# Kernel tuning notes

Hardware: AMD Instinct MI355X
Metric: run time of the kernel (lower is better)

The kernel has to match this reference:

```python
import jax, jax.numpy as jnp
import numpy as np

ALPHA = 1.702   # GLU sigmoid scale
LIMIT = 7.0     # clamp limit
K = 2           # experts per token


def setup_inputs() -> dict:
    key = jax.random.key(0)
    ks = jax.random.split(key, 4)
    B, S, H, E, I = 1, 1024, 1024, 8, 1024
    return {
        "hidden_states": jax.random.normal(ks[0], (B, S, H), jnp.float32),
        "router_weight": jax.random.normal(ks[1], (E, H), jnp.float32),
        "router_bias": jnp.zeros((E,), jnp.float32),
        "gate_up_proj": jax.random.normal(ks[2], (E, H, 2 * I), jnp.float32) * 0.02,
        "gate_up_bias": jnp.zeros((E, 2 * I), jnp.float32),
        "down_proj": jax.random.normal(ks[3], (E, I, H), jnp.float32) * 0.02,
        "down_bias": jnp.zeros((E, H), jnp.float32),
    }


def reference(hidden_states, router_weight, router_bias, gate_up_proj,
              gate_up_bias, down_proj, down_bias):
    B, S, H = hidden_states.shape
    E = router_weight.shape[0]
    I = down_proj.shape[1]
    T = B * S

    flat = hidden_states.reshape(T, H)

    # Router: softmax over experts, top-K selection (weights NOT renormalized).
    logits = flat @ router_weight.T + router_bias               # [T, E]
    scores = jax.nn.softmax(logits, axis=-1)
    topk_vals, topk_idx = jax.lax.top_k(scores, K)              # [T, K]

    # Dense per-token expert weight matrix (equivalent of dispatch metadata +
    # combine * topk_weights in the tt pipeline); top-k indices are unique.
    w = jnp.zeros((T, E), scores.dtype).at[
        jnp.arange(T)[:, None], topk_idx].set(topk_vals)        # [T, E]

    # Expert MLP with clamped GLU (gpt-oss style).
    gu = jnp.einsum('th,ehf->tef', flat, gate_up_proj) + gate_up_bias  # [T,E,2I]
    gate = jnp.minimum(gu[..., :I], LIMIT)
    up = jnp.clip(gu[..., I:], -LIMIT, LIMIT)
    glu = gate * jax.nn.sigmoid(gate * ALPHA)
    act = (up + 1.0) * glu                                       # [T, E, I]

    down = jnp.einsum('tei,eih->teh', act, down_proj) + down_bias  # [T, E, H]

    # Weighted combine over selected experts.
    out = jnp.einsum('teh,te->th', down, w)
    return out.reshape(B, S, H)
```

## Files before the change

kernel.cpp:

```cpp
#include <hip/hip_runtime.h>
#include <hip/hip_bf16.h>


typedef unsigned short u16;
typedef __attribute__((ext_vector_type(8))) __bf16 bf16x8;
typedef __attribute__((ext_vector_type(4))) float f32x4;

#define T_TOK 1024
#define H_DIM 1024
#define E_NUM 8
#define I_DIM 1024
#define ALPHA 1.702f
#define LIMIT 7.0f

__device__ __forceinline__ u16 f2bf(float f) {
    unsigned u = __builtin_bit_cast(unsigned, f);
    u = (u + 0x7FFFu + ((u >> 16) & 1u)) >> 16;
    return (u16)u;
}

__device__ __forceinline__ unsigned pk2(float lo, float hi) {
#if defined(__has_builtin) && __has_builtin(__builtin_amdgcn_cvt_pk_bf16_f32)
    typedef __attribute__((ext_vector_type(2))) __bf16 bf16x2_t;
    bf16x2_t v = __builtin_amdgcn_cvt_pk_bf16_f32(lo, hi);
    return __builtin_bit_cast(unsigned, v);
#else
    return (unsigned)f2bf(lo) | ((unsigned)f2bf(hi) << 16);
#endif
}

__device__ __forceinline__ f32x4 mfma16(bf16x8 a, bf16x8 b, f32x4 c) {
    return __builtin_amdgcn_mfma_f32_16x16x32_bf16(a, b, c, 0, 0, 0);
}

__device__ __forceinline__ void gld16(const void* g, void* l) {
    __builtin_amdgcn_global_load_lds(
        (const __attribute__((address_space(1))) void*)g,
        (__attribute__((address_space(3))) void*)l, 16, 0, 0);
}

__device__ __forceinline__ void expert_range(const int* counts, int e,
                                             int& cnt, int& abase) {
    int a = 0, c = 0;
#pragma unroll
    for (int i = 0; i < E_NUM; ++i) {
        int v = counts[i];
        if (i < e) a += v;
        if (i == e) c = v;
    }
    cnt = c; abase = a;
}

__global__ __launch_bounds__(256) void k_cvt(
    const float* __restrict__ gup, const float* __restrict__ dp,
    u16* __restrict__ gupT, u16* __restrict__ dpT, int* __restrict__ counts)
{
    if (blockIdx.x == 0 && threadIdx.x < E_NUM) counts[threadIdx.x] = 0;
    const int b = blockIdx.x;
    const float* src; u16* dst; int C, k0, c0;
    if (b < 4096) {
        int e = b >> 9, t = b & 511;
        k0 = (t >> 5) * 64; c0 = (t & 31) * 64;
        src = gup + ((size_t)e << 21); dst = gupT + ((size_t)e << 21); C = 2048;
    } else {
        int b2 = b - 4096;
        int e = b2 >> 8, t = b2 & 255;
        k0 = (t >> 4) * 64; c0 = (t & 15) * 64;
        src = dp + ((size_t)e << 20); dst = dpT + ((size_t)e << 20); C = 1024;
    }
    __shared__ __align__(16) u16 Ls[64][72];
    const int tid = threadIdx.x;
    const int kq = tid >> 4, cq = tid & 15;
    float4 v0 = *(const float4*)(src + (size_t)(k0 + kq * 4 + 0) * C + c0 + cq * 4);
    float4 v1 = *(const float4*)(src + (size_t)(k0 + kq * 4 + 1) * C + c0 + cq * 4);
    float4 v2 = *(const float4*)(src + (size_t)(k0 + kq * 4 + 2) * C + c0 + cq * 4);
    float4 v3 = *(const float4*)(src + (size_t)(k0 + kq * 4 + 3) * C + c0 + cq * 4);
    const float* p0 = (const float*)&v0; const float* p1 = (const float*)&v1;
    const float* p2 = (const float*)&v2; const float* p3 = (const float*)&v3;
#pragma unroll
    for (int i = 0; i < 4; ++i) {
        *(uint2*)&Ls[cq * 4 + i][kq * 4] =
            make_uint2(pk2(p0[i], p1[i]), pk2(p2[i], p3[i]));
    }
    __syncthreads();
    const int oc = tid >> 2, och = (tid & 3) * 16;
    u16* orow = dst + (size_t)(c0 + oc) * 1024 + k0 + och;
    *(uint4*)(orow)     = *(uint4*)&Ls[oc][och];
    *(uint4*)(orow + 8) = *(uint4*)&Ls[oc][och + 8];
}

__global__ __launch_bounds__(256) void k_router(
    const float* __restrict__ x, const float* __restrict__ rw,
    const float* __restrict__ rb, const float* __restrict__ db,
    int* __restrict__ counts, int* __restrict__ tok_list,
    float* __restrict__ w_list, u16* __restrict__ xb,
    float* __restrict__ out)
{
    const int t = blockIdx.x;
    const int tid = threadIdx.x;
    const float4 xv = *(const float4*)(x + (size_t)t * H_DIM + tid * 4);

    *(uint2*)(xb + (size_t)t * H_DIM + tid * 4) =
        make_uint2(pk2(xv.x, xv.y), pk2(xv.z, xv.w));

    float p[E_NUM];
#pragma unroll
    for (int e = 0; e < E_NUM; ++e) {
        const float4 wv = *(const float4*)(rw + e * H_DIM + tid * 4);
        p[e] = xv.x * wv.x + xv.y * wv.y + xv.z * wv.z + xv.w * wv.w;
    }
#pragma unroll
    for (int off = 32; off; off >>= 1) {
#pragma unroll
        for (int e = 0; e < E_NUM; ++e) p[e] += __shfl_down(p[e], off, 64);
    }
    __shared__ float red[4][E_NUM];
    __shared__ int se[2];
    __shared__ float sw[2];
    const int lane = tid & 63, wvid = tid >> 6;
    if (lane == 0) {
#pragma unroll
        for (int e = 0; e < E_NUM; ++e) red[wvid][e] = p[e];
    }
    __syncthreads();
    if (tid == 0) {
        float lg[E_NUM];
#pragma unroll
        for (int e = 0; e < E_NUM; ++e)
            lg[e] = red[0][e] + red[1][e] + red[2][e] + red[3][e] + rb[e];
        float m1 = -1e30f, m2 = -1e30f; int i1 = 0, i2 = 0;
#pragma unroll
        for (int e = 0; e < E_NUM; ++e) {
            float l = lg[e];
            if (l > m1) { m2 = m1; i2 = i1; m1 = l; i1 = e; }
            else if (l > m2) { m2 = l; i2 = e; }
        }
        float s = 0.f;
#pragma unroll
        for (int e = 0; e < E_NUM; ++e) s += __expf(lg[e] - m1);
        const float w0 = 1.0f / s;
        const float w1 = __expf(m2 - m1) / s;
        int slot0 = atomicAdd(&counts[i1], 1);
        tok_list[i1 * T_TOK + slot0] = t;
        w_list[i1 * T_TOK + slot0] = w0;
        int slot1 = atomicAdd(&counts[i2], 1);
        tok_list[i2 * T_TOK + slot1] = t;
        w_list[i2 * T_TOK + slot1] = w1;
        se[0] = i1; se[1] = i2; sw[0] = w0; sw[1] = w1;
    }
    __syncthreads();
    const int e0 = se[0], e1 = se[1];
    const float w0 = sw[0], w1 = sw[1];
    const int c = tid * 4;
    float4 d0 = *(const float4*)(db + e0 * H_DIM + c);
    float4 d1 = *(const float4*)(db + e1 * H_DIM + c);
    float4 o;
    o.x = w0 * d0.x + w1 * d1.x;
    o.y = w0 * d0.y + w1 * d1.y;
    o.z = w0 * d0.z + w1 * d1.z;
    o.w = w0 * d0.w + w1 * d1.w;
    *(float4*)(out + (size_t)t * H_DIM + c) = o;
}

__global__ __launch_bounds__(256, 3) void k_gateup(
    const u16* __restrict__ gupT, const float* __restrict__ gub,
    const int* __restrict__ counts, const int* __restrict__ tok_list,
    const u16* __restrict__ xb, u16* __restrict__ act)
{
    const int e = blockIdx.z;
    int cnt, abase;
    expert_range(counts, e, cnt, abase);
    const int m0 = blockIdx.y * 64;
    if (m0 >= cnt) return;
    const int n0 = blockIdx.x * 64;
    const int tid = threadIdx.x;
    const int lane = tid & 63, wv = tid >> 6;
    const int fm = lane & 15, kg = lane >> 4;
    const int wm = wv >> 1, wn = wv & 1;

    __shared__ __align__(16) u16 As0[64 * 64], As1[64 * 64];
    __shared__ __align__(16) u16 Bs0[128 * 64], Bs1[128 * 64];

    const int lr = lane >> 3, lk = (lane & 7) * 8;
    const u16* gA[2];
#pragma unroll
    for (int i = 0; i < 2; ++i) {
        int row = (wv * 2 + i) * 8 + lr;
        int slot = m0 + row;
        int tok = (slot < cnt) ? tok_list[e * T_TOK + slot] : 0;
        gA[i] = xb + (size_t)tok * H_DIM + lk;
    }
    const u16* gB[4];
#pragma unroll
    for (int i = 0; i < 4; ++i) {
        int row = (wv * 4 + i) * 8 + lr;
        int col = (row < 64) ? (n0 + row) : (1024 + n0 + row - 64);
        gB[i] = gupT + ((size_t)e << 21) + (size_t)col * 1024 + lk;
    }

    f32x4 accg[2][2], accu[2][2];
#pragma unroll
    for (int m = 0; m < 2; ++m)
#pragma unroll
        for (int n = 0; n < 2; ++n) {
            accg[m][n] = (f32x4){0.f, 0.f, 0.f, 0.f};
            accu[m][n] = (f32x4){0.f, 0.f, 0.f, 0.f};
        }

#define GU_STAGE(AS, BS, KB)                                                   \
    {                                                                          \
        gld16(gA[0] + (KB), (u16*)(AS) + (wv * 2 + 0) * 512);                  \
        gld16(gA[1] + (KB), (u16*)(AS) + (wv * 2 + 1) * 512);                  \
        gld16(gB[0] + (KB), (u16*)(BS) + (wv * 4 + 0) * 512);                  \
        gld16(gB[1] + (KB), (u16*)(BS) + (wv * 4 + 1) * 512);                  \
        gld16(gB[2] + (KB), (u16*)(BS) + (wv * 4 + 2) * 512);                  \
        gld16(gB[3] + (KB), (u16*)(BS) + (wv * 4 + 3) * 512);                  \
    }
#define GU_MFMA(AS, BS)                                                        \
    {                                                                          \
        _Pragma("unroll")                                                      \
        for (int ks = 0; ks < 2; ++ks) {                                       \
            const int ko = ks * 32 + kg * 8;                                   \
            bf16x8 a0 = *(const bf16x8*)((const u16*)(AS) + (wm * 32 + fm) * 64 + ko);        \
            bf16x8 a1 = *(const bf16x8*)((const u16*)(AS) + (wm * 32 + 16 + fm) * 64 + ko);   \
            bf16x8 bg0 = *(const bf16x8*)((const u16*)(BS) + (wn * 32 + fm) * 64 + ko);       \
            bf16x8 bg1 = *(const bf16x8*)((const u16*)(BS) + (wn * 32 + 16 + fm) * 64 + ko);  \
            bf16x8 bu0 = *(const bf16x8*)((const u16*)(BS) + (64 + wn * 32 + fm) * 64 + ko);  \
            bf16x8 bu1 = *(const bf16x8*)((const u16*)(BS) + (64 + wn * 32 + 16 + fm) * 64 + ko); \
            accg[0][0] = mfma16(a0, bg0, accg[0][0]);                          \
            accg[0][1] = mfma16(a0, bg1, accg[0][1]);                          \
            accu[0][0] = mfma16(a0, bu0, accu[0][0]);                          \
            accu[0][1] = mfma16(a0, bu1, accu[0][1]);                          \
            accg[1][0] = mfma16(a1, bg0, accg[1][0]);                          \
            accg[1][1] = mfma16(a1, bg1, accg[1][1]);                          \
            accu[1][0] = mfma16(a1, bu0, accu[1][0]);                          \
            accu[1][1] = mfma16(a1, bu1, accu[1][1]);                          \
        }                                                                      \
    }

    GU_STAGE(As0, Bs0, 0);
    __syncthreads();
    for (int kb = 0; kb < H_DIM; kb += 128) {
        GU_STAGE(As1, Bs1, kb + 64);
        GU_MFMA(As0, Bs0);
        __syncthreads();
        if (kb + 128 < H_DIM) GU_STAGE(As0, Bs0, kb + 128);
        GU_MFMA(As1, Bs1);
        __syncthreads();
    }
#undef GU_STAGE
#undef GU_MFMA

#pragma unroll
    for (int m = 0; m < 2; ++m) {
#pragma unroll
        for (int r = 0; r < 4; ++r) {
            int row = wm * 32 + m * 16 + kg * 4 + r;
            int slot = m0 + row;
            if (slot >= cnt) continue;
            size_t arow = (size_t)(abase + slot) * I_DIM;
#pragma unroll
            for (int n = 0; n < 2; ++n) {
                int cn = n0 + wn * 32 + n * 16 + fm;
                float g = accg[m][n][r] + gub[e * 2048 + cn];
                float u = accu[m][n][r] + gub[e * 2048 + 1024 + cn];
                g = fminf(g, LIMIT);
                u = fminf(fmaxf(u, -LIMIT), LIMIT);
                float glu = g / (1.f + __expf(-ALPHA * g));
                act[arow + cn] = f2bf((u + 1.f) * glu);
            }
        }
    }
}

__global__ __launch_bounds__(256, 4) void k_down(
    const u16* __restrict__ dpT,
    const int* __restrict__ counts, const int* __restrict__ tok_list,
    const float* __restrict__ w_list,
    const u16* __restrict__ act, float* __restrict__ out)
{
    const int e = blockIdx.z;
    int cnt, abase;
    expert_range(counts, e, cnt, abase);
    const int m0 = blockIdx.y * 64;
    if (m0 >= cnt) return;
    const int n0 = blockIdx.x * 64;
    const int tid = threadIdx.x;
    const int lane = tid & 63, wv = tid >> 6;
    const int fm = lane & 15, kg = lane >> 4;
    const int wm = wv >> 1, wn = wv & 1;

    __shared__ __align__(16) u16 As0[64 * 64], As1[64 * 64];
    __shared__ __align__(16) u16 Bs0[64 * 64], Bs1[64 * 64];

    const int lr = lane >> 3, lk = (lane & 7) * 8;
    const u16* gA[2];
    const u16* gB[2];
#pragma unroll
    for (int i = 0; i < 2; ++i) {
        int row = (wv * 2 + i) * 8 + lr;
        gA[i] = act + (size_t)(abase + m0 + row) * I_DIM + lk;
        gB[i] = dpT + ((size_t)e << 20) + (size_t)(n0 + row) * 1024 + lk;
    }

    f32x4 acc[2][2];
#pragma unroll
    for (int m = 0; m < 2; ++m)
#pragma unroll
        for (int n = 0; n < 2; ++n) acc[m][n] = (f32x4){0.f, 0.f, 0.f, 0.f};

#define DN_STAGE(AS, BS, KB)                                                   \
    {                                                                          \
        gld16(gA[0] + (KB), (u16*)(AS) + (wv * 2 + 0) * 512);                  \
        gld16(gA[1] + (KB), (u16*)(AS) + (wv * 2 + 1) * 512);                  \
        gld16(gB[0] + (KB), (u16*)(BS) + (wv * 2 + 0) * 512);                  \
        gld16(gB[1] + (KB), (u16*)(BS) + (wv * 2 + 1) * 512);                  \
    }
#define DN_MFMA(AS, BS)                                                        \
    {                                                                          \
        _Pragma("unroll")                                                      \
        for (int ks2 = 0; ks2 < 2; ++ks2) {                                    \
            const int ko = ks2 * 32 + kg * 8;                                  \
            bf16x8 a0 = *(const bf16x8*)((const u16*)(AS) + (wm * 32 + fm) * 64 + ko);      \
            bf16x8 a1 = *(const bf16x8*)((const u16*)(AS) + (wm * 32 + 16 + fm) * 64 + ko); \
            bf16x8 b0 = *(const bf16x8*)((const u16*)(BS) + (wn * 32 + fm) * 64 + ko);      \
            bf16x8 b1 = *(const bf16x8*)((const u16*)(BS) + (wn * 32 + 16 + fm) * 64 + ko); \
            acc[0][0] = mfma16(a0, b0, acc[0][0]);                             \
            acc[0][1] = mfma16(a0, b1, acc[0][1]);                             \
            acc[1][0] = mfma16(a1, b0, acc[1][0]);                             \
            acc[1][1] = mfma16(a1, b1, acc[1][1]);                             \
        }                                                                      \
    }

    DN_STAGE(As0, Bs0, 0);
    __syncthreads();
    for (int kb = 0; kb < I_DIM; kb += 128) {
        DN_STAGE(As1, Bs1, kb + 64);
        DN_MFMA(As0, Bs0);
        __syncthreads();
        if (kb + 128 < I_DIM) DN_STAGE(As0, Bs0, kb + 128);
        DN_MFMA(As1, Bs1);
        __syncthreads();
    }
#undef DN_STAGE
#undef DN_MFMA

#pragma unroll
    for (int m = 0; m < 2; ++m) {
#pragma unroll
        for (int r = 0; r < 4; ++r) {
            int row = wm * 32 + m * 16 + kg * 4 + r;
            int slot = m0 + row;
            if (slot >= cnt) continue;
            float wgt = w_list[e * T_TOK + slot];
            int tok = tok_list[e * T_TOK + slot];
            float* orow = out + (size_t)tok * H_DIM;
#pragma unroll
            for (int n = 0; n < 2; ++n) {
                int col = n0 + wn * 32 + n * 16 + fm;
                atomicAdd(orow + col, acc[m][n][r] * wgt);
            }
        }
    }
}

extern "C" void kernel_launch(void* const* d_in, const int* in_sizes, int n_in,
                              void* d_out, int out_size, void* d_ws, size_t ws_size,
                              hipStream_t stream) {
    const float* x   = (const float*)d_in[0];
    const float* rw  = (const float*)d_in[1];
    const float* rb  = (const float*)d_in[2];
    const float* gup = (const float*)d_in[3];
    const float* gub = (const float*)d_in[4];
    const float* dp  = (const float*)d_in[5];
    const float* db  = (const float*)d_in[6];
    float* out = (float*)d_out;

    char* ws = (char*)d_ws;
    int*   counts   = (int*)(ws);
    int*   tok_list = (int*)(ws + 64);
    float* w_list   = (float*)(ws + 64 + 32768);
    u16*   xb       = (u16*)(ws + 65600);
    u16*   act      = (u16*)(ws + 65600 + 2097152);
    u16*   gupT     = (u16*)(ws + 8388608);
    u16*   dpT      = (u16*)(ws + 41943040);

    k_cvt<<<6144, 256, 0, stream>>>(gup, dp, gupT, dpT, counts);
    k_router<<<T_TOK, 256, 0, stream>>>(x, rw, rb, db, counts, tok_list, w_list,
                                        xb, out);
    k_gateup<<<dim3(16, 16, 8), 256, 0, stream>>>(gupT, gub, counts, tok_list,
                                                  xb, act);
    k_down<<<dim3(16, 16, 8), 256, 0, stream>>>(dpT, counts, tok_list, w_list,
                                                act, out);
}
```

Measured before the change: 216.1 us.

## Triple-buffer LDS with explicit vmcnt waits and XOR-swizzle in both expert GEMMs

Replaces the double-buffered K loop in the gate-up and down GEMMs with a three-stage LDS ring. Two tiles stay in flight, and hand-placed s_waitcnt vmcnt counts plus a single barrier per step replace the two __syncthreads per iteration. It also XOR-swizzles the 16-byte column chunk on both the global-to-LDS load and the MFMA fragment read, to cut LDS bank conflicts. In exchange, the extra LDS buffer lowers the launch-bounds occupancy hint for both kernels and makes correctness depend on the hand-computed outstanding-load counts.

Result: faster. 207.5 us (-4.0%).

```diff
diff --git a/kernel.cpp b/kernel.cpp
--- a/kernel.cpp
+++ b/kernel.cpp
@@ -162,7 +162,7 @@
     *(float4*)(out + (size_t)t * H_DIM + c) = o;
 }
 
-__global__ __launch_bounds__(256, 3) void k_gateup(
+__global__ __launch_bounds__(256, 2) void k_gateup(
     const u16* __restrict__ gupT, const float* __restrict__ gub,
     const int* __restrict__ counts, const int* __restrict__ tok_list,
     const u16* __restrict__ xb, u16* __restrict__ act)
@@ -178,10 +178,13 @@
     const int fm = lane & 15, kg = lane >> 4;
     const int wm = wv >> 1, wn = wv & 1;
 
-    __shared__ __align__(16) u16 As0[64 * 64], As1[64 * 64];
-    __shared__ __align__(16) u16 Bs0[128 * 64], Bs1[128 * 64];
-
-    const int lr = lane >> 3, lk = (lane & 7) * 8;
+    __shared__ __align__(16) u16 As0[64 * 64], As1[64 * 64], As2[64 * 64];
+    __shared__ __align__(16) u16 Bs0[128 * 64], Bs1[128 * 64], Bs2[128 * 64];
+    u16* const AB[3] = {As0, As1, As2};
+    u16* const BB[3] = {Bs0, Bs1, Bs2};
+
+    const int lr = lane >> 3;
+    const int lk = ((lane & 7) ^ lr) * 8;
     const u16* gA[2];
 #pragma unroll
     for (int i = 0; i < 2; ++i) {
@@ -220,7 +223,7 @@
     {                                                                          \
         _Pragma("unroll")                                                      \
         for (int ks = 0; ks < 2; ++ks) {                                       \
-            const int ko = ks * 32 + kg * 8;                                   \
+            const int ko = (((ks * 4 + kg) ^ (fm & 7)) << 3);                  \
             bf16x8 a0 = *(const bf16x8*)((const u16*)(AS) + (wm * 32 + fm) * 64 + ko);        \
             bf16x8 a1 = *(const bf16x8*)((const u16*)(AS) + (wm * 32 + 16 + fm) * 64 + ko);   \
             bf16x8 bg0 = *(const bf16x8*)((const u16*)(BS) + (wn * 32 + fm) * 64 + ko);       \
@@ -238,15 +241,15 @@
         }                                                                      \
     }
 
-    GU_STAGE(As0, Bs0, 0);
-    __syncthreads();
-    for (int kb = 0; kb < H_DIM; kb += 128) {
-        GU_STAGE(As1, Bs1, kb + 64);
-        GU_MFMA(As0, Bs0);
-        __syncthreads();
-        if (kb + 128 < H_DIM) GU_STAGE(As0, Bs0, kb + 128);
-        GU_MFMA(As1, Bs1);
-        __syncthreads();
+    GU_STAGE(AB[0], BB[0], 0);
+    GU_STAGE(AB[1], BB[1], 64);
+#pragma unroll
+    for (int p = 0; p < 16; ++p) {
+        if (p == 15) { asm volatile("s_waitcnt vmcnt(0) lgkmcnt(0)" ::: "memory"); }
+        else         { asm volatile("s_waitcnt vmcnt(6) lgkmcnt(0)" ::: "memory"); }
+        __builtin_amdgcn_s_barrier();
+        if (p + 2 < 16) GU_STAGE(AB[(p + 2) % 3], BB[(p + 2) % 3], (p + 2) * 64);
+        GU_MFMA(AB[p % 3], BB[p % 3]);
     }
 #undef GU_STAGE
 #undef GU_MFMA
@@ -273,7 +276,7 @@
     }
 }
 
-__global__ __launch_bounds__(256, 4) void k_down(
+__global__ __launch_bounds__(256, 3) void k_down(
     const u16* __restrict__ dpT,
     const int* __restrict__ counts, const int* __restrict__ tok_list,
     const float* __restrict__ w_list,
@@ -290,10 +293,13 @@
     const int fm = lane & 15, kg = lane >> 4;
     const int wm = wv >> 1, wn = wv & 1;
 
-    __shared__ __align__(16) u16 As0[64 * 64], As1[64 * 64];
-    __shared__ __align__(16) u16 Bs0[64 * 64], Bs1[64 * 64];
-
-    const int lr = lane >> 3, lk = (lane & 7) * 8;
+    __shared__ __align__(16) u16 As0[64 * 64], As1[64 * 64], As2[64 * 64];
+    __shared__ __align__(16) u16 Bs0[64 * 64], Bs1[64 * 64], Bs2[64 * 64];
+    u16* const AB[3] = {As0, As1, As2};
+    u16* const BB[3] = {Bs0, Bs1, Bs2};
+
+    const int lr = lane >> 3;
+    const int lk = ((lane & 7) ^ lr) * 8;
     const u16* gA[2];
     const u16* gB[2];
 #pragma unroll
@@ -319,8 +325,8 @@
 #define DN_MFMA(AS, BS)                                                        \
     {                                                                          \
         _Pragma("unroll")                                                      \
-        for (int ks2 = 0; ks2 < 2; ++ks2) {                                    \
-            const int ko = ks2 * 32 + kg * 8;                                  \
+        for (int ks = 0; ks < 2; ++ks) {                                       \
+            const int ko = (((ks * 4 + kg) ^ (fm & 7)) << 3);                  \
             bf16x8 a0 = *(const bf16x8*)((const u16*)(AS) + (wm * 32 + fm) * 64 + ko);      \
             bf16x8 a1 = *(const bf16x8*)((const u16*)(AS) + (wm * 32 + 16 + fm) * 64 + ko); \
             bf16x8 b0 = *(const bf16x8*)((const u16*)(BS) + (wn * 32 + fm) * 64 + ko);      \
@@ -332,15 +338,15 @@
         }                                                                      \
     }
 
-    DN_STAGE(As0, Bs0, 0);
-    __syncthreads();
-    for (int kb = 0; kb < I_DIM; kb += 128) {
-        DN_STAGE(As1, Bs1, kb + 64);
-        DN_MFMA(As0, Bs0);
-        __syncthreads();
-        if (kb + 128 < I_DIM) DN_STAGE(As0, Bs0, kb + 128);
-        DN_MFMA(As1, Bs1);
-        __syncthreads();
+    DN_STAGE(AB[0], BB[0], 0);
+    DN_STAGE(AB[1], BB[1], 64);
+#pragma unroll
+    for (int p = 0; p < 16; ++p) {
+        if (p == 15) { asm volatile("s_waitcnt vmcnt(0) lgkmcnt(0)" ::: "memory"); }
+        else         { asm volatile("s_waitcnt vmcnt(4) lgkmcnt(0)" ::: "memory"); }
+        __builtin_amdgcn_s_barrier();
+        if (p + 2 < 16) DN_STAGE(AB[(p + 2) % 3], BB[(p + 2) % 3], (p + 2) * 64);
+        DN_MFMA(AB[p % 3], BB[p % 3]);
     }
 #undef DN_STAGE
 #undef DN_MFMA
```

## Fuse fp32-to-bf16 weight conversion into expert GEMM tile loads

Applied to the files above, without the earlier changes.

Drops the separate weight transpose/convert pass, which read all fp32 expert weights and wrote bf16 transposed copies. The gate-up and down GEMMs now load fp32 weights straight from global memory into registers, pack them to bf16 and write them transposed into padded LDS tiles, using a three-stage register prefetch pipeline with explicit waitcnt and barriers. This removes a full extra write and read of the weights. In exchange, each GEMM block re-reads fp32 weights at twice the bytes, some of them several times across token tiles, uses more registers (gate-up occupancy hint lowered to 2), and gives up direct global-to-LDS loads.

New measurement: 228.0 us. 1.05x slower.

```diff
diff --git a/kernel.cpp b/kernel.cpp
--- a/kernel.cpp
+++ b/kernel.cpp
@@ -33,12 +33,6 @@
     return __builtin_amdgcn_mfma_f32_16x16x32_bf16(a, b, c, 0, 0, 0);
 }
 
-__device__ __forceinline__ void gld16(const void* g, void* l) {
-    __builtin_amdgcn_global_load_lds(
-        (const __attribute__((address_space(1))) void*)g,
-        (__attribute__((address_space(3))) void*)l, 16, 0, 0);
-}
-
 __device__ __forceinline__ void expert_range(const int* counts, int e,
                                              int& cnt, int& abase) {
     int a = 0, c = 0;
@@ -51,42 +45,8 @@
     cnt = c; abase = a;
 }
 
-__global__ __launch_bounds__(256) void k_cvt(
-    const float* __restrict__ gup, const float* __restrict__ dp,
-    u16* __restrict__ gupT, u16* __restrict__ dpT, int* __restrict__ counts)
-{
-    if (blockIdx.x == 0 && threadIdx.x < E_NUM) counts[threadIdx.x] = 0;
-    const int b = blockIdx.x;
-    const float* src; u16* dst; int C, k0, c0;
-    if (b < 4096) {
-        int e = b >> 9, t = b & 511;
-        k0 = (t >> 5) * 64; c0 = (t & 31) * 64;
-        src = gup + ((size_t)e << 21); dst = gupT + ((size_t)e << 21); C = 2048;
-    } else {
-        int b2 = b - 4096;
-        int e = b2 >> 8, t = b2 & 255;
-        k0 = (t >> 4) * 64; c0 = (t & 15) * 64;
-        src = dp + ((size_t)e << 20); dst = dpT + ((size_t)e << 20); C = 1024;
-    }
-    __shared__ __align__(16) u16 Ls[64][72];
-    const int tid = threadIdx.x;
-    const int kq = tid >> 4, cq = tid & 15;
-    float4 v0 = *(const float4*)(src + (size_t)(k0 + kq * 4 + 0) * C + c0 + cq * 4);
-    float4 v1 = *(const float4*)(src + (size_t)(k0 + kq * 4 + 1) * C + c0 + cq * 4);
-    float4 v2 = *(const float4*)(src + (size_t)(k0 + kq * 4 + 2) * C + c0 + cq * 4);
-    float4 v3 = *(const float4*)(src + (size_t)(k0 + kq * 4 + 3) * C + c0 + cq * 4);
-    const float* p0 = (const float*)&v0; const float* p1 = (const float*)&v1;
-    const float* p2 = (const float*)&v2; const float* p3 = (const float*)&v3;
-#pragma unroll
-    for (int i = 0; i < 4; ++i) {
-        *(uint2*)&Ls[cq * 4 + i][kq * 4] =
-            make_uint2(pk2(p0[i], p1[i]), pk2(p2[i], p3[i]));
-    }
-    __syncthreads();
-    const int oc = tid >> 2, och = (tid & 3) * 16;
-    u16* orow = dst + (size_t)(c0 + oc) * 1024 + k0 + och;
-    *(uint4*)(orow)     = *(uint4*)&Ls[oc][och];
-    *(uint4*)(orow + 8) = *(uint4*)&Ls[oc][och + 8];
+__global__ void k_zero(int* counts) {
+    if (threadIdx.x < E_NUM) counts[threadIdx.x] = 0;
 }
 
 __global__ __launch_bounds__(256) void k_router(
@@ -162,8 +122,8 @@
     *(float4*)(out + (size_t)t * H_DIM + c) = o;
 }
 
-__global__ __launch_bounds__(256, 3) void k_gateup(
-    const u16* __restrict__ gupT, const float* __restrict__ gub,
+__global__ __launch_bounds__(256, 2) void k_gateup(
+    const float* __restrict__ gup, const float* __restrict__ gub,
     const int* __restrict__ counts, const int* __restrict__ tok_list,
     const u16* __restrict__ xb, u16* __restrict__ act)
 {
@@ -178,25 +138,19 @@
     const int fm = lane & 15, kg = lane >> 4;
     const int wm = wv >> 1, wn = wv & 1;
 
-    __shared__ __align__(16) u16 As0[64 * 64], As1[64 * 64];
-    __shared__ __align__(16) u16 Bs0[128 * 64], Bs1[128 * 64];
-
-    const int lr = lane >> 3, lk = (lane & 7) * 8;
-    const u16* gA[2];
-#pragma unroll
-    for (int i = 0; i < 2; ++i) {
-        int row = (wv * 2 + i) * 8 + lr;
-        int slot = m0 + row;
-        int tok = (slot < cnt) ? tok_list[e * T_TOK + slot] : 0;
-        gA[i] = xb + (size_t)tok * H_DIM + lk;
-    }
-    const u16* gB[4];
-#pragma unroll
-    for (int i = 0; i < 4; ++i) {
-        int row = (wv * 4 + i) * 8 + lr;
-        int col = (row < 64) ? (n0 + row) : (1024 + n0 + row - 64);
-        gB[i] = gupT + ((size_t)e << 21) + (size_t)col * 1024 + lk;
-    }
+    __shared__ __align__(16) u16 As[2][64 * 72];
+    __shared__ __align__(16) u16 Bs[2][128 * 72];
+    unsigned* const Bs32[2] = {(unsigned*)Bs[0], (unsigned*)Bs[1]};
+
+    const int kq = tid >> 3, cq = tid & 7;
+    const int arow = tid >> 2, kc = tid & 3;
+    const int aslot = m0 + arow;
+    const int atok = (aslot < cnt) ? tok_list[e * T_TOK + aslot] : 0;
+    const u16* gA = xb + (size_t)atok * H_DIM;
+    const float* gB = gup + ((size_t)e << 21) + n0;
+
+    float4 Bf[2][2][2][2];
+    uint4 Aa[2][2];
 
     f32x4 accg[2][2], accu[2][2];
 #pragma unroll
@@ -207,26 +161,47 @@
             accu[m][n] = (f32x4){0.f, 0.f, 0.f, 0.f};
         }
 
-#define GU_STAGE(AS, BS, KB)                                                   \
-    {                                                                          \
-        gld16(gA[0] + (KB), (u16*)(AS) + (wv * 2 + 0) * 512);                  \
-        gld16(gA[1] + (KB), (u16*)(AS) + (wv * 2 + 1) * 512);                  \
-        gld16(gB[0] + (KB), (u16*)(BS) + (wv * 4 + 0) * 512);                  \
-        gld16(gB[1] + (KB), (u16*)(BS) + (wv * 4 + 1) * 512);                  \
-        gld16(gB[2] + (KB), (u16*)(BS) + (wv * 4 + 2) * 512);                  \
-        gld16(gB[3] + (KB), (u16*)(BS) + (wv * 4 + 3) * 512);                  \
-    }
-#define GU_MFMA(AS, BS)                                                        \
+#define GU_LOADS(S, KB)                                                        \
+    {                                                                          \
+        _Pragma("unroll")                                                      \
+        for (int sub = 0; sub < 2; ++sub)                                      \
+        _Pragma("unroll")                                                      \
+        for (int half = 0; half < 2; ++half)                                   \
+        _Pragma("unroll")                                                      \
+        for (int j = 0; j < 2; ++j)                                            \
+            Bf[S][sub][half][j] = *(const float4*)(gB +                        \
+                (size_t)((KB) + 2 * kq + j) * 2048 + half * 1024 +             \
+                sub * 32 + cq * 4);                                            \
+        Aa[S][0] = *(const uint4*)(gA + (KB) + kc * 16);                       \
+        Aa[S][1] = *(const uint4*)(gA + (KB) + kc * 16 + 8);                   \
+    }
+#define GU_WRITE(S, BUF)                                                       \
+    {                                                                          \
+        _Pragma("unroll")                                                      \
+        for (int sub = 0; sub < 2; ++sub)                                      \
+        _Pragma("unroll")                                                      \
+        for (int half = 0; half < 2; ++half)                                   \
+        _Pragma("unroll")                                                      \
+        for (int c = 0; c < 4; ++c) {                                          \
+            const float* j0 = (const float*)&Bf[S][sub][half][0];              \
+            const float* j1 = (const float*)&Bf[S][sub][half][1];              \
+            Bs32[BUF][(half * 64 + sub * 32 + cq * 4 + c) * 36 + kq] =         \
+                pk2(j0[c], j1[c]);                                             \
+        }                                                                      \
+        *(uint4*)&As[BUF][arow * 72 + kc * 16]     = Aa[S][0];                 \
+        *(uint4*)&As[BUF][arow * 72 + kc * 16 + 8] = Aa[S][1];                 \
+    }
+#define GU_MFMA(BUF)                                                           \
     {                                                                          \
         _Pragma("unroll")                                                      \
         for (int ks = 0; ks < 2; ++ks) {                                       \
             const int ko = ks * 32 + kg * 8;                                   \
-            bf16x8 a0 = *(const bf16x8*)((const u16*)(AS) + (wm * 32 + fm) * 64 + ko);        \
-            bf16x8 a1 = *(const bf16x8*)((const u16*)(AS) + (wm * 32 + 16 + fm) * 64 + ko);   \
-            bf16x8 bg0 = *(const bf16x8*)((const u16*)(BS) + (wn * 32 + fm) * 64 + ko);       \
-            bf16x8 bg1 = *(const bf16x8*)((const u16*)(BS) + (wn * 32 + 16 + fm) * 64 + ko);  \
-            bf16x8 bu0 = *(const bf16x8*)((const u16*)(BS) + (64 + wn * 32 + fm) * 64 + ko);  \
-            bf16x8 bu1 = *(const bf16x8*)((const u16*)(BS) + (64 + wn * 32 + 16 + fm) * 64 + ko); \
+            bf16x8 a0 = *(const bf16x8*)&As[BUF][(wm * 32 + fm) * 72 + ko];        \
+            bf16x8 a1 = *(const bf16x8*)&As[BUF][(wm * 32 + 16 + fm) * 72 + ko];   \
+            bf16x8 bg0 = *(const bf16x8*)&Bs[BUF][(wn * 32 + fm) * 72 + ko];       \
+            bf16x8 bg1 = *(const bf16x8*)&Bs[BUF][(wn * 32 + 16 + fm) * 72 + ko];  \
+            bf16x8 bu0 = *(const bf16x8*)&Bs[BUF][(64 + wn * 32 + fm) * 72 + ko];  \
+            bf16x8 bu1 = *(const bf16x8*)&Bs[BUF][(64 + wn * 32 + 16 + fm) * 72 + ko]; \
             accg[0][0] = mfma16(a0, bg0, accg[0][0]);                          \
             accg[0][1] = mfma16(a0, bg1, accg[0][1]);                          \
             accu[0][0] = mfma16(a0, bu0, accu[0][0]);                          \
@@ -238,17 +213,28 @@
         }                                                                      \
     }
 
-    GU_STAGE(As0, Bs0, 0);
-    __syncthreads();
-    for (int kb = 0; kb < H_DIM; kb += 128) {
-        GU_STAGE(As1, Bs1, kb + 64);
-        GU_MFMA(As0, Bs0);
-        __syncthreads();
-        if (kb + 128 < H_DIM) GU_STAGE(As0, Bs0, kb + 128);
-        GU_MFMA(As1, Bs1);
-        __syncthreads();
-    }
-#undef GU_STAGE
+    GU_LOADS(0, 0);
+    GU_LOADS(1, 64);
+    asm volatile("s_waitcnt vmcnt(10)" ::: "memory");
+    GU_WRITE(0, 0);
+    GU_LOADS(0, 128);
+    asm volatile("s_waitcnt lgkmcnt(0)" ::: "memory");
+    __builtin_amdgcn_s_barrier();
+
+#pragma unroll
+    for (int t = 0; t < 16; ++t) {
+        if (t <= 13)      { asm volatile("s_waitcnt vmcnt(10)" ::: "memory"); }
+        else if (t == 14) { asm volatile("s_waitcnt vmcnt(0)"  ::: "memory"); }
+        if (t + 1 < 16) GU_WRITE((t + 1) & 1, (t + 1) & 1);
+        if (t + 3 < 16) GU_LOADS((t + 3) & 1, (t + 3) * 64);
+        GU_MFMA(t & 1);
+        if (t + 1 < 16) {
+            asm volatile("s_waitcnt lgkmcnt(0)" ::: "memory");
+            __builtin_amdgcn_s_barrier();
+        }
+    }
+#undef GU_LOADS
+#undef GU_WRITE
 #undef GU_MFMA
 
 #pragma unroll
@@ -258,7 +244,7 @@
             int row = wm * 32 + m * 16 + kg * 4 + r;
             int slot = m0 + row;
             if (slot >= cnt) continue;
-            size_t arow = (size_t)(abase + slot) * I_DIM;
+            size_t arowo = (size_t)(abase + slot) * I_DIM;
 #pragma unroll
             for (int n = 0; n < 2; ++n) {
                 int cn = n0 + wn * 32 + n * 16 + fm;
@@ -267,14 +253,14 @@
                 g = fminf(g, LIMIT);
                 u = fminf(fmaxf(u, -LIMIT), LIMIT);
                 float glu = g / (1.f + __expf(-ALPHA * g));
-                act[arow + cn] = f2bf((u + 1.f) * glu);
+                act[arowo + cn] = f2bf((u + 1.f) * glu);
             }
         }
     }
 }
 
 __global__ __launch_bounds__(256, 4) void k_down(
-    const u16* __restrict__ dpT,
+    const float* __restrict__ dp,
     const int* __restrict__ counts, const int* __restrict__ tok_list,
     const float* __restrict__ w_list,
     const u16* __restrict__ act, float* __restrict__ out)
@@ -290,18 +276,17 @@
     const int fm = lane & 15, kg = lane >> 4;
     const int wm = wv >> 1, wn = wv & 1;
 
-    __shared__ __align__(16) u16 As0[64 * 64], As1[64 * 64];
-    __shared__ __align__(16) u16 Bs0[64 * 64], Bs1[64 * 64];
-
-    const int lr = lane >> 3, lk = (lane & 7) * 8;
-    const u16* gA[2];
-    const u16* gB[2];
-#pragma unroll
-    for (int i = 0; i < 2; ++i) {
-        int row = (wv * 2 + i) * 8 + lr;
-        gA[i] = act + (size_t)(abase + m0 + row) * I_DIM + lk;
-        gB[i] = dpT + ((size_t)e << 20) + (size_t)(n0 + row) * 1024 + lk;
-    }
+    __shared__ __align__(16) u16 As[2][64 * 72];
+    __shared__ __align__(16) u16 Bs[2][64 * 72];
+    unsigned* const Bs32[2] = {(unsigned*)Bs[0], (unsigned*)Bs[1]};
+
+    const int kq = tid >> 3, cq = tid & 7;
+    const int arow = tid >> 2, kc = tid & 3;
+    const u16* gA = act + (size_t)(abase + m0 + arow) * I_DIM;
+    const float* gB = dp + ((size_t)e << 20) + n0;
+
+    float4 Bf[2][2][2];
+    uint4 Aa[2][2];
 
     f32x4 acc[2][2];
 #pragma unroll
@@ -309,22 +294,39 @@
 #pragma unroll
         for (int n = 0; n < 2; ++n) acc[m][n] = (f32x4){0.f, 0.f, 0.f, 0.f};
 
-#define DN_STAGE(AS, BS, KB)                                                   \
-    {                                                                          \
-        gld16(gA[0] + (KB), (u16*)(AS) + (wv * 2 + 0) * 512);                  \
-        gld16(gA[1] + (KB), (u16*)(AS) + (wv * 2 + 1) * 512);                  \
-        gld16(gB[0] + (KB), (u16*)(BS) + (wv * 2 + 0) * 512);                  \
-        gld16(gB[1] + (KB), (u16*)(BS) + (wv * 2 + 1) * 512);                  \
-    }
-#define DN_MFMA(AS, BS)                                                        \
-    {                                                                          \
-        _Pragma("unroll")                                                      \
-        for (int ks2 = 0; ks2 < 2; ++ks2) {                                    \
-            const int ko = ks2 * 32 + kg * 8;                                  \
-            bf16x8 a0 = *(const bf16x8*)((const u16*)(AS) + (wm * 32 + fm) * 64 + ko);      \
-            bf16x8 a1 = *(const bf16x8*)((const u16*)(AS) + (wm * 32 + 16 + fm) * 64 + ko); \
-            bf16x8 b0 = *(const bf16x8*)((const u16*)(BS) + (wn * 32 + fm) * 64 + ko);      \
-            bf16x8 b1 = *(const bf16x8*)((const u16*)(BS) + (wn * 32 + 16 + fm) * 64 + ko); \
+#define DN_LOADS(S, KB)                                                        \
+    {                                                                          \
+        _Pragma("unroll")                                                      \
+        for (int sub = 0; sub < 2; ++sub)                                      \
+        _Pragma("unroll")                                                      \
+        for (int j = 0; j < 2; ++j)                                            \
+            Bf[S][sub][j] = *(const float4*)(gB +                              \
+                (size_t)((KB) + 2 * kq + j) * 1024 + sub * 32 + cq * 4);       \
+        Aa[S][0] = *(const uint4*)(gA + (KB) + kc * 16);                       \
+        Aa[S][1] = *(const uint4*)(gA + (KB) + kc * 16 + 8);                   \
+    }
+#define DN_WRITE(S, BUF)                                                       \
+    {                                                                          \
+        _Pragma("unroll")                                                      \
+        for (int sub = 0; sub < 2; ++sub)                                      \
+        _Pragma("unroll")                                                      \
+        for (int c = 0; c < 4; ++c) {                                          \
+            const float* j0 = (const float*)&Bf[S][sub][0];                    \
+            const float* j1 = (const float*)&Bf[S][sub][1];                    \
+            Bs32[BUF][(sub * 32 + cq * 4 + c) * 36 + kq] = pk2(j0[c], j1[c]);  \
+        }                                                                      \
+        *(uint4*)&As[BUF][arow * 72 + kc * 16]     = Aa[S][0];                 \
+        *(uint4*)&As[BUF][arow * 72 + kc * 16 + 8] = Aa[S][1];                 \
+    }
+#define DN_MFMA(BUF)                                                           \
+    {                                                                          \
+        _Pragma("unroll")                                                      \
+        for (int ks = 0; ks < 2; ++ks) {                                       \
+            const int ko = ks * 32 + kg * 8;                                   \
+            bf16x8 a0 = *(const bf16x8*)&As[BUF][(wm * 32 + fm) * 72 + ko];      \
+            bf16x8 a1 = *(const bf16x8*)&As[BUF][(wm * 32 + 16 + fm) * 72 + ko]; \
+            bf16x8 b0 = *(const bf16x8*)&Bs[BUF][(wn * 32 + fm) * 72 + ko];      \
+            bf16x8 b1 = *(const bf16x8*)&Bs[BUF][(wn * 32 + 16 + fm) * 72 + ko]; \
             acc[0][0] = mfma16(a0, b0, acc[0][0]);                             \
             acc[0][1] = mfma16(a0, b1, acc[0][1]);                             \
             acc[1][0] = mfma16(a1, b0, acc[1][0]);                             \
@@ -332,17 +334,28 @@
         }                                                                      \
     }
 
-    DN_STAGE(As0, Bs0, 0);
-    __syncthreads();
-    for (int kb = 0; kb < I_DIM; kb += 128) {
-        DN_STAGE(As1, Bs1, kb + 64);
-        DN_MFMA(As0, Bs0);
-        __syncthreads();
-        if (kb + 128 < I_DIM) DN_STAGE(As0, Bs0, kb + 128);
-        DN_MFMA(As1, Bs1);
-        __syncthreads();
-    }
-#undef DN_STAGE
+    DN_LOADS(0, 0);
+    DN_LOADS(1, 64);
+    asm volatile("s_waitcnt vmcnt(6)" ::: "memory");
+    DN_WRITE(0, 0);
+    DN_LOADS(0, 128);
+    asm volatile("s_waitcnt lgkmcnt(0)" ::: "memory");
+    __builtin_amdgcn_s_barrier();
+
+#pragma unroll
+    for (int t = 0; t < 16; ++t) {
+        if (t <= 13)      { asm volatile("s_waitcnt vmcnt(6)" ::: "memory"); }
+        else if (t == 14) { asm volatile("s_waitcnt vmcnt(0)" ::: "memory"); }
+        if (t + 1 < 16) DN_WRITE((t + 1) & 1, (t + 1) & 1);
+        if (t + 3 < 16) DN_LOADS((t + 3) & 1, (t + 3) * 64);
+        DN_MFMA(t & 1);
+        if (t + 1 < 16) {
+            asm volatile("s_waitcnt lgkmcnt(0)" ::: "memory");
+            __builtin_amdgcn_s_barrier();
+        }
+    }
+#undef DN_LOADS
+#undef DN_WRITE
 #undef DN_MFMA
 
 #pragma unroll
@@ -382,14 +395,12 @@
     float* w_list   = (float*)(ws + 64 + 32768);
     u16*   xb       = (u16*)(ws + 65600);
     u16*   act      = (u16*)(ws + 65600 + 2097152);
-    u16*   gupT     = (u16*)(ws + 8388608);
-    u16*   dpT      = (u16*)(ws + 41943040);
-
-    k_cvt<<<6144, 256, 0, stream>>>(gup, dp, gupT, dpT, counts);
+
+    k_zero<<<1, 64, 0, stream>>>(counts);
     k_router<<<T_TOK, 256, 0, stream>>>(x, rw, rb, db, counts, tok_list, w_list,
                                         xb, out);
-    k_gateup<<<dim3(16, 16, 8), 256, 0, stream>>>(gupT, gub, counts, tok_list,
+    k_gateup<<<dim3(16, 16, 8), 256, 0, stream>>>(gup, gub, counts, tok_list,
                                                   xb, act);
-    k_down<<<dim3(16, 16, 8), 256, 0, stream>>>(dpT, counts, tok_list, w_list,
+    k_down<<<dim3(16, 16, 8), 256, 0, stream>>>(dp, counts, tok_list, w_list,
                                                 act, out);
 }
```
